# Optimization experiments

Hardware: AMD Instinct MI355X
Metric: run time of the kernel (lower is better)

Reference implementation:

```python
import jax, jax.numpy as jnp
import numpy as np

B, L, H, E = 2, 2048, 16, 64  # self-attention: S=L, D=E


def setup_inputs() -> dict:
    key = jax.random.key(0)
    kq, kk, kv = jax.random.split(key, 3)
    queries = jax.random.normal(kq, (B, L, H, E), dtype=jnp.float32)
    keys = jax.random.normal(kk, (B, L, H, E), dtype=jnp.float32)
    values = jax.random.normal(kv, (B, L, H, E), dtype=jnp.float32)
    return {"queries": queries, "keys": keys, "values": values}


def reference(queries, keys, values):
    # Faithful to source: scale is computed in torch code but never applied.
    # scores: [B, H, L, S]
    scores = jnp.einsum("blhe,bshe->bhls", queries, keys)
    # TriangularCausalMask: triu(ones, diagonal=1) -> mask strictly-future positions
    Lq = queries.shape[1]
    causal = jnp.triu(jnp.ones((Lq, Lq), dtype=bool), k=1)  # [L, S]
    scores = jnp.where(causal[None, None, :, :], -jnp.inf, scores)
    A = jax.nn.softmax(scores, axis=-1)  # dropout in eval mode = identity
    V = jnp.einsum("bhls,bshd->blhd", A, values)
    return V
```

## Files before the change

kernel.cpp:

```cpp
#include <hip/hip_runtime.h>

typedef short bf16x8 __attribute__((ext_vector_type(8)));
typedef short bf16x4 __attribute__((ext_vector_type(4)));
typedef short bf16x2 __attribute__((ext_vector_type(2)));
typedef float f32x4 __attribute__((ext_vector_type(4)));

#define LOG2E 1.4426950408889634f

static __device__ __forceinline__ unsigned short f2bf(float x) {
  unsigned int u = __builtin_bit_cast(unsigned int, x);
  u += 0x7fffu + ((u >> 16) & 1u);
  return (unsigned short)(u >> 16);
}
static __device__ __forceinline__ float bf2f(unsigned short h) {
  unsigned int u = ((unsigned int)h) << 16;
  return __builtin_bit_cast(float, u);
}

static __device__ __forceinline__ void gl_lds16(const void* g, void* l) {
  __builtin_amdgcn_global_load_lds(
      (const __attribute__((address_space(1))) void*)g,
      (__attribute__((address_space(3))) void*)l, 16, 0, 0);
}

__global__ __launch_bounds__(256)
void prep_kv(const float* __restrict__ K, const float* __restrict__ V,
             short* __restrict__ ws) {
  __shared__ float tmp[64 * 65];
  const int isV = blockIdx.x >> 10;
  const int tile = blockIdx.x & 1023;
  const int bh = tile >> 5, kt = tile & 31;
  const int b = bh >> 4, h = bh & 15;
  const int tid = threadIdx.x;
  if (!isV) {
    const float* Kb = K + ((size_t)b * 2048 + kt * 64) * 1024 + h * 64;
    short* ohi = ws + (size_t)tile * 4096;
    short* olo = ws + 4194304 + (size_t)tile * 4096;
    for (int i = 0; i < 2; ++i) {
      const int chunk = tid + 256 * i;
      const int row = chunk >> 3, p = chunk & 7;
      const int c = p ^ (row & 7);
      const float* src = Kb + (size_t)row * 1024 + c * 8;
      const f32x4 a = *(const f32x4*)src;
      const f32x4 d = *(const f32x4*)(src + 4);
      bf16x8 hi, lo;
      for (int j = 0; j < 4; ++j) {
        const unsigned short hb = f2bf(a[j]);
        hi[j] = (short)hb; lo[j] = (short)f2bf(a[j] - bf2f(hb));
      }
      for (int j = 0; j < 4; ++j) {
        const unsigned short hb = f2bf(d[j]);
        hi[4 + j] = (short)hb; lo[4 + j] = (short)f2bf(d[j] - bf2f(hb));
      }
      *(bf16x8*)(ohi + chunk * 8) = hi;
      *(bf16x8*)(olo + chunk * 8) = lo;
    }
  } else {
    const float* Vb = V + ((size_t)b * 2048 + kt * 64) * 1024 + h * 64;
    short* ovt = ws + 8388608 + (size_t)tile * 4096;
    for (int i = 0; i < 4; ++i) {
      const int idx = tid + 256 * i;
      const int row = idx >> 4, c4 = idx & 15;
      const f32x4 v = *(const f32x4*)(Vb + (size_t)row * 1024 + c4 * 4);
      for (int j = 0; j < 4; ++j) tmp[row * 65 + c4 * 4 + j] = v[j];
    }
    __syncthreads();
    for (int i = 0; i < 2; ++i) {
      const int chunk = tid + 256 * i;
      const int e = chunk >> 3, p = chunk & 7;
      const int s0 = (p ^ (e & 7)) * 8;
      bf16x8 o;
      for (int j = 0; j < 8; ++j) o[j] = (short)f2bf(tmp[(s0 + j) * 65 + e]);
      *(bf16x8*)(ovt + chunk * 8) = o;
    }
  }
}

__global__ __launch_bounds__(256, 2)
void fa_fwd2(const float* __restrict__ Qg, const short* __restrict__ ws,
             float* __restrict__ Og) {
  __shared__ short sKhi[2][4096];
  __shared__ short sKlo[2][4096];
  __shared__ short sVt[2][4096];
  __shared__ short sP[4096];

  const int tid = threadIdx.x;
  const int lane = tid & 63;
  const int wv = tid >> 6;
  const int ml = lane & 15, quad = lane >> 4;
  const int bh = blockIdx.x;
  const int b = bh >> 4, h = bh & 15;
  const float* Qb = Qg + (size_t)b * 2048 * 1024 + h * 64;
  float* Ob = Og + (size_t)b * 2048 * 1024 + h * 64;
  const short* wsKhi = ws;
  const short* wsKlo = ws + 4194304;
  const short* wsVt = ws + 8388608;
  const int wrow0 = wv * 16;
  const bf16x8 ones = {16256, 16256, 16256, 16256, 16256, 16256, 16256, 16256};
  const f32x4 vzero = {0.f, 0.f, 0.f, 0.f};

  for (int half = 0; half < 2; ++half) {
    const int qt = half ? 31 - (int)blockIdx.y : (int)blockIdx.y;
    const int qbase = qt * 64;
    const int nkt = qt + 1;

    bf16x8 qhi[2], qlo[2];
    {
      const float* qr = Qb + (size_t)(qbase + wrow0 + ml) * 1024;
      for (int ks = 0; ks < 2; ++ks) {
        const int e0 = ks * 32 + quad * 8;
        const f32x4 a = *(const f32x4*)(qr + e0);
        const f32x4 c4 = *(const f32x4*)(qr + e0 + 4);
        for (int j = 0; j < 4; ++j) {
          const unsigned short hb = f2bf(a[j]);
          qhi[ks][j] = (short)hb;
          qlo[ks][j] = (short)f2bf(a[j] - bf2f(hb));
        }
        for (int j = 0; j < 4; ++j) {
          const unsigned short hb = f2bf(c4[j]);
          qhi[ks][4 + j] = (short)hb;
          qlo[ks][4 + j] = (short)f2bf(c4[j] - bf2f(hb));
        }
      }
    }

    f32x4 acc[4];
    f32x4 accl = vzero;
    for (int et = 0; et < 4; ++et) acc[et] = vzero;

    auto stage = [&](int kt, int bf) {
      const size_t ktile = ((size_t)bh * 32 + kt) * 4096;
      const short* g0 = wsKhi + ktile;
      const short* g1 = wsKlo + ktile;
      const short* g2 = wsVt + ktile;
      const int o0 = tid * 8, o1 = (tid + 256) * 8;
      gl_lds16(g0 + o0, &sKhi[bf][o0]);
      gl_lds16(g0 + o1, &sKhi[bf][o1]);
      gl_lds16(g1 + o0, &sKlo[bf][o0]);
      gl_lds16(g1 + o1, &sKlo[bf][o1]);
      gl_lds16(g2 + o0, &sVt[bf][o0]);
      gl_lds16(g2 + o1, &sVt[bf][o1]);
    };

    stage(0, 0);
    __syncthreads();

    for (int kt = 0; kt < nkt; ++kt) {
      const int buf = kt & 1;
      if (kt + 1 < nkt) stage(kt + 1, buf ^ 1);

      f32x4 S[4];
      for (int nt = 0; nt < 4; ++nt) S[nt] = vzero;
      for (int ks = 0; ks < 2; ++ks) {
        const int ch = (ks << 2) + quad;
        for (int nt = 0; nt < 4; ++nt) {
          const int srow = nt * 16 + ml;
          const int off = srow * 64 + ((ch ^ (srow & 7)) << 3);
          const bf16x8 kh = *(const bf16x8*)(&sKhi[buf][off]);
          const bf16x8 kl = *(const bf16x8*)(&sKlo[buf][off]);
          S[nt] = __builtin_amdgcn_mfma_f32_16x16x32_bf16(qhi[ks], kh, S[nt], 0, 0, 0);
          S[nt] = __builtin_amdgcn_mfma_f32_16x16x32_bf16(qlo[ks], kh, S[nt], 0, 0, 0);
          S[nt] = __builtin_amdgcn_mfma_f32_16x16x32_bf16(qhi[ks], kl, S[nt], 0, 0, 0);
        }
      }

      const bool dg = (kt * 64 + 63) > (qbase + wrow0);
      for (int nt = 0; nt < 4; ++nt)
        for (int r = 0; r < 4; ++r) {
          float p = __builtin_amdgcn_exp2f(S[nt][r] * LOG2E);
          if (dg) {
            const int sg = kt * 64 + nt * 16 + ml;
            const int lg = qbase + wrow0 + quad * 4 + r;
            if (sg > lg) p = 0.f;
          }
          const int pr = wrow0 + quad * 4 + r;
          const int s = nt * 16 + ml;
          sP[pr * 64 + (((s >> 3) ^ (pr & 7)) << 3) + (s & 7)] = (short)f2bf(p);
        }

      for (int ks = 0; ks < 2; ++ks) {
        const int ch = (ks << 2) + quad;
        const int lrow = wrow0 + ml;
        const bf16x8 pa = *(const bf16x8*)(&sP[lrow * 64 + ((ch ^ (lrow & 7)) << 3)]);
        accl = __builtin_amdgcn_mfma_f32_16x16x32_bf16(pa, ones, accl, 0, 0, 0);
        for (int et = 0; et < 4; ++et) {
          const int e = et * 16 + ml;
          const bf16x8 vb = *(const bf16x8*)(&sVt[buf][e * 64 + ((ch ^ (e & 7)) << 3)]);
          acc[et] = __builtin_amdgcn_mfma_f32_16x16x32_bf16(pa, vb, acc[et], 0, 0, 0);
        }
      }
      __syncthreads();
    }

    for (int r = 0; r < 4; ++r) {
      const float inv = 1.0f / accl[r];
      float* orow = Ob + (size_t)(qbase + wrow0 + quad * 4 + r) * 1024;
      for (int et = 0; et < 4; ++et)
        orow[et * 16 + ml] = acc[et][r] * inv;
    }
  }
}

__global__ __launch_bounds__(512, 2)
void fa_fwd_fb(const float* __restrict__ Qg, const float* __restrict__ Kg,
               const float* __restrict__ Vg, float* __restrict__ Og) {
  constexpr int HE = 1024, Lr = 2048;
  __shared__ short sKhi[2][64 * 64];
  __shared__ short sKlo[2][64 * 64];
  __shared__ short sVt[2][64 * 64];
  __shared__ short sP[128 * 64];

  const int tid = threadIdx.x;
  const int lane = tid & 63;
  const int wv = tid >> 6;
  const int ml = lane & 15;
  const int quad = lane >> 4;

  const int b = blockIdx.x >> 4, h = blockIdx.x & 15;
  const size_t headoff = (size_t)b * (size_t)Lr * HE + (size_t)h * 64;
  const float* Qb = Qg + headoff;
  const float* Kb = Kg + headoff;
  const float* Vb = Vg + headoff;
  float* Ob = Og + headoff;

  const f32x4 vzero = {0.f, 0.f, 0.f, 0.f};

  for (int half = 0; half < 2; ++half) {
    const int qt = half ? (15 - (int)blockIdx.y) : (int)blockIdx.y;
    const int qbase = qt * 128;
    const int wrow0 = wv * 16;

    bf16x8 qhi[2], qlo[2];
    {
      const float* qr = Qb + (size_t)(qbase + wrow0 + ml) * HE;
      for (int ks = 0; ks < 2; ++ks) {
        const int e0 = ks * 32 + quad * 8;
        const f32x4 a = *(const f32x4*)(qr + e0);
        const f32x4 c4 = *(const f32x4*)(qr + e0 + 4);
        for (int j = 0; j < 4; ++j) {
          const unsigned short hb = f2bf(a[j]);
          qhi[ks][j] = (short)hb;
          qlo[ks][j] = (short)f2bf(a[j] - bf2f(hb));
        }
        for (int j = 0; j < 4; ++j) {
          const unsigned short hb = f2bf(c4[j]);
          qhi[ks][4 + j] = (short)hb;
          qlo[ks][4 + j] = (short)f2bf(c4[j] - bf2f(hb));
        }
      }
    }

    f32x4 acc[4];
    float mrun[4], lrun[4];
    for (int et = 0; et < 4; ++et) acc[et] = vzero;
    for (int r = 0; r < 4; ++r) { mrun[r] = -1e30f; lrun[r] = 0.f; }

    const int nkt = 2 * qt + 2;
    for (int kt = 0; kt < nkt; ++kt) {
      const int buf = kt & 1;
      for (int i = 0; i < 2; ++i) {
        const int idx = tid + 512 * i;
        const int row = idx >> 4, c = idx & 15;
        const f32x4 kv = *(const f32x4*)(Kb + (size_t)(kt * 64 + row) * HE + c * 4);
        bf16x4 hi, lo;
        for (int j = 0; j < 4; ++j) {
          const unsigned short hb = f2bf(kv[j]);
          hi[j] = (short)hb;
          lo[j] = (short)f2bf(kv[j] - bf2f(hb));
        }
        const int off = row * 64 + (((c >> 1) ^ (row & 7)) << 3) + ((c & 1) << 2);
        *(bf16x4*)(&sKhi[buf][off]) = hi;
        *(bf16x4*)(&sKlo[buf][off]) = lo;
      }
      {
        const int c = tid & 15, rb = tid >> 4;
        const int s0 = rb * 2;
        const f32x4 v0 = *(const f32x4*)(Vb + (size_t)(kt * 64 + s0) * HE + c * 4);
        const f32x4 v1 = *(const f32x4*)(Vb + (size_t)(kt * 64 + s0 + 1) * HE + c * 4);
        for (int j = 0; j < 4; ++j) {
          const int e = c * 4 + j;
          bf16x2 p;
          p[0] = (short)f2bf(v0[j]);
          p[1] = (short)f2bf(v1[j]);
          const int off = e * 64 + (((s0 >> 3) ^ (e & 7)) << 3) + (s0 & 7);
          *(bf16x2*)(&sVt[buf][off]) = p;
        }
      }
      __syncthreads();

      f32x4 S[4];
      for (int nt = 0; nt < 4; ++nt) S[nt] = vzero;
      for (int ks = 0; ks < 2; ++ks) {
        const int ch = (ks << 2) + quad;
        for (int nt = 0; nt < 4; ++nt) {
          const int srow = nt * 16 + ml;
          const int off = srow * 64 + ((ch ^ (srow & 7)) << 3);
          const bf16x8 kh = *(const bf16x8*)(&sKhi[buf][off]);
          const bf16x8 kl = *(const bf16x8*)(&sKlo[buf][off]);
          S[nt] = __builtin_amdgcn_mfma_f32_16x16x32_bf16(qhi[ks], kh, S[nt], 0, 0, 0);
          S[nt] = __builtin_amdgcn_mfma_f32_16x16x32_bf16(qlo[ks], kh, S[nt], 0, 0, 0);
          S[nt] = __builtin_amdgcn_mfma_f32_16x16x32_bf16(qhi[ks], kl, S[nt], 0, 0, 0);
        }
      }

      if (kt * 64 + 63 > qbase + wrow0) {
        for (int nt = 0; nt < 4; ++nt)
          for (int r = 0; r < 4; ++r) {
            const int sg = kt * 64 + nt * 16 + ml;
            const int lg = qbase + wrow0 + quad * 4 + r;
            if (sg > lg) S[nt][r] = -1e30f;
          }
      }

      float mnew[4], al[4], rsum[4];
      for (int r = 0; r < 4; ++r) {
        float mx = fmaxf(fmaxf(S[0][r], S[1][r]), fmaxf(S[2][r], S[3][r]));
        mx = fmaxf(mx, __shfl_xor(mx, 1));
        mx = fmaxf(mx, __shfl_xor(mx, 2));
        mx = fmaxf(mx, __shfl_xor(mx, 4));
        mx = fmaxf(mx, __shfl_xor(mx, 8));
        mnew[r] = fmaxf(mrun[r], mx);
        al[r] = __builtin_amdgcn_exp2f((mrun[r] - mnew[r]) * LOG2E);
        mrun[r] = mnew[r];
        rsum[r] = 0.f;
      }
      for (int nt = 0; nt < 4; ++nt)
        for (int r = 0; r < 4; ++r) {
          const float p = __builtin_amdgcn_exp2f((S[nt][r] - mnew[r]) * LOG2E);
          S[nt][r] = p;
          rsum[r] += p;
        }
      for (int r = 0; r < 4; ++r) {
        rsum[r] += __shfl_xor(rsum[r], 1);
        rsum[r] += __shfl_xor(rsum[r], 2);
        rsum[r] += __shfl_xor(rsum[r], 4);
        rsum[r] += __shfl_xor(rsum[r], 8);
        lrun[r] = lrun[r] * al[r] + rsum[r];
      }
      for (int et = 0; et < 4; ++et)
        for (int r = 0; r < 4; ++r) acc[et][r] *= al[r];

      for (int nt = 0; nt < 4; ++nt)
        for (int r = 0; r < 4; ++r) {
          const int pr = wrow0 + quad * 4 + r;
          const int s = nt * 16 + ml;
          sP[pr * 64 + (((s >> 3) ^ (pr & 7)) << 3) + (s & 7)] = (short)f2bf(S[nt][r]);
        }

      for (int ks = 0; ks < 2; ++ks) {
        const int ch = (ks << 2) + quad;
        const int lrow = wrow0 + ml;
        const bf16x8 pa = *(const bf16x8*)(&sP[lrow * 64 + ((ch ^ (lrow & 7)) << 3)]);
        for (int et = 0; et < 4; ++et) {
          const int e = et * 16 + ml;
          const bf16x8 vb = *(const bf16x8*)(&sVt[buf][e * 64 + ((ch ^ (e & 7)) << 3)]);
          acc[et] = __builtin_amdgcn_mfma_f32_16x16x32_bf16(pa, vb, acc[et], 0, 0, 0);
        }
      }
    }

    for (int r = 0; r < 4; ++r) {
      const float inv = 1.0f / lrun[r];
      float* orow = Ob + (size_t)(qbase + wrow0 + quad * 4 + r) * HE;
      for (int et = 0; et < 4; ++et)
        orow[et * 16 + ml] = acc[et][r] * inv;
    }
  }
}

extern "C" void kernel_launch(void* const* d_in, const int* in_sizes, int n_in,
                              void* d_out, int out_size, void* d_ws, size_t ws_size,
                              hipStream_t stream) {
  const float* Q = (const float*)d_in[0];
  const float* K = (const float*)d_in[1];
  const float* V = (const float*)d_in[2];
  float* O = (float*)d_out;
  if (ws_size >= 25165824u) {
    short* ws = (short*)d_ws;
    hipLaunchKernelGGL(prep_kv, dim3(2048, 1, 1), dim3(256, 1, 1), 0, stream, K, V, ws);
    hipLaunchKernelGGL(fa_fwd2, dim3(32, 16, 1), dim3(256, 1, 1), 0, stream, Q, ws, O);
  } else {
    hipLaunchKernelGGL(fa_fwd_fb, dim3(32, 8, 1), dim3(512, 1, 1), 0, stream, Q, K, V, O);
  }
}
```

Measured before the change: 144.0 us.

## Give each wave two 16-row query tiles and each block one 128-row tile

The new attention kernel assigns one 128-row query tile per block, with each wave computing two 16-row m-tiles. Each K and V fragment read from LDS now feeds twice as many MFMAs, which cuts LDS traffic and halves K/V staging per query row. It drops the old pairing of tiles qt and 31-qt, so per-block work now ranges from 2 to 32 key tiles. With all blocks resident at once, the heaviest blocks may lengthen the critical path. It also doubles the sP scratch buffer and raises register pressure.

```diff
diff --git a/kernel.cpp b/kernel.cpp
--- a/kernel.cpp
+++ b/kernel.cpp
@@ -77,12 +77,12 @@
 }
 
 __global__ __launch_bounds__(256, 2)
-void fa_fwd2(const float* __restrict__ Qg, const short* __restrict__ ws,
+void fa_fwd3(const float* __restrict__ Qg, const short* __restrict__ ws,
              float* __restrict__ Og) {
   __shared__ short sKhi[2][4096];
   __shared__ short sKlo[2][4096];
   __shared__ short sVt[2][4096];
-  __shared__ short sP[4096];
+  __shared__ short sP[8192];
 
   const int tid = threadIdx.x;
   const int lane = tid & 63;
@@ -95,18 +95,155 @@
   const short* wsKhi = ws;
   const short* wsKlo = ws + 4194304;
   const short* wsVt = ws + 8388608;
-  const int wrow0 = wv * 16;
+  const int wrow0 = wv * 32;
   const bf16x8 ones = {16256, 16256, 16256, 16256, 16256, 16256, 16256, 16256};
   const f32x4 vzero = {0.f, 0.f, 0.f, 0.f};
 
+  const int qt = 15 - (int)blockIdx.y;
+  const int qbase = qt * 128;
+  const int nkt = 2 * qt + 2;
+
+  bf16x8 qhi[2][2], qlo[2][2];
+  for (int mt = 0; mt < 2; ++mt) {
+    const float* qr = Qb + (size_t)(qbase + wrow0 + mt * 16 + ml) * 1024;
+    for (int ks = 0; ks < 2; ++ks) {
+      const int e0 = ks * 32 + quad * 8;
+      const f32x4 a = *(const f32x4*)(qr + e0);
+      const f32x4 c4 = *(const f32x4*)(qr + e0 + 4);
+      for (int j = 0; j < 4; ++j) {
+        const unsigned short hb = f2bf(a[j]);
+        qhi[mt][ks][j] = (short)hb;
+        qlo[mt][ks][j] = (short)f2bf(a[j] - bf2f(hb));
+      }
+      for (int j = 0; j < 4; ++j) {
+        const unsigned short hb = f2bf(c4[j]);
+        qhi[mt][ks][4 + j] = (short)hb;
+        qlo[mt][ks][4 + j] = (short)f2bf(c4[j] - bf2f(hb));
+      }
+    }
+  }
+
+  f32x4 acc[2][4];
+  f32x4 accl[2];
+  for (int mt = 0; mt < 2; ++mt) {
+    accl[mt] = vzero;
+    for (int et = 0; et < 4; ++et) acc[mt][et] = vzero;
+  }
+
+  auto stage = [&](int kt, int bf) {
+    const size_t ktile = ((size_t)bh * 32 + kt) * 4096;
+    const short* g0 = wsKhi + ktile;
+    const short* g1 = wsKlo + ktile;
+    const short* g2 = wsVt + ktile;
+    const int o0 = tid * 8, o1 = (tid + 256) * 8;
+    gl_lds16(g0 + o0, &sKhi[bf][o0]);
+    gl_lds16(g0 + o1, &sKhi[bf][o1]);
+    gl_lds16(g1 + o0, &sKlo[bf][o0]);
+    gl_lds16(g1 + o1, &sKlo[bf][o1]);
+    gl_lds16(g2 + o0, &sVt[bf][o0]);
+    gl_lds16(g2 + o1, &sVt[bf][o1]);
+  };
+
+  stage(0, 0);
+  __syncthreads();
+
+  for (int kt = 0; kt < nkt; ++kt) {
+    const int buf = kt & 1;
+    if (kt + 1 < nkt) stage(kt + 1, buf ^ 1);
+
+    f32x4 S[2][4];
+    for (int mt = 0; mt < 2; ++mt)
+      for (int nt = 0; nt < 4; ++nt) S[mt][nt] = vzero;
+    for (int ks = 0; ks < 2; ++ks) {
+      const int ch = (ks << 2) + quad;
+      for (int nt = 0; nt < 4; ++nt) {
+        const int srow = nt * 16 + ml;
+        const int off = srow * 64 + ((ch ^ (srow & 7)) << 3);
+        const bf16x8 kh = *(const bf16x8*)(&sKhi[buf][off]);
+        const bf16x8 kl = *(const bf16x8*)(&sKlo[buf][off]);
+        for (int mt = 0; mt < 2; ++mt) {
+          S[mt][nt] = __builtin_amdgcn_mfma_f32_16x16x32_bf16(qhi[mt][ks], kh, S[mt][nt], 0, 0, 0);
+          S[mt][nt] = __builtin_amdgcn_mfma_f32_16x16x32_bf16(qlo[mt][ks], kh, S[mt][nt], 0, 0, 0);
+          S[mt][nt] = __builtin_amdgcn_mfma_f32_16x16x32_bf16(qhi[mt][ks], kl, S[mt][nt], 0, 0, 0);
+        }
+      }
+    }
+
+    for (int mt = 0; mt < 2; ++mt) {
+      const bool dg = (kt * 64 + 63) > (qbase + wrow0 + mt * 16);
+      for (int nt = 0; nt < 4; ++nt)
+        for (int r = 0; r < 4; ++r) {
+          float p = __builtin_amdgcn_exp2f(S[mt][nt][r] * LOG2E);
+          if (dg) {
+            const int sg = kt * 64 + nt * 16 + ml;
+            const int lg = qbase + wrow0 + mt * 16 + quad * 4 + r;
+            if (sg > lg) p = 0.f;
+          }
+          const int pr = wrow0 + mt * 16 + quad * 4 + r;
+          const int s = nt * 16 + ml;
+          sP[pr * 64 + (((s >> 3) ^ (pr & 7)) << 3) + (s & 7)] = (short)f2bf(p);
+        }
+    }
+
+    for (int ks = 0; ks < 2; ++ks) {
+      const int ch = (ks << 2) + quad;
+      bf16x8 pa[2];
+      for (int mt = 0; mt < 2; ++mt) {
+        const int lrow = wrow0 + mt * 16 + ml;
+        pa[mt] = *(const bf16x8*)(&sP[lrow * 64 + ((ch ^ (lrow & 7)) << 3)]);
+        accl[mt] = __builtin_amdgcn_mfma_f32_16x16x32_bf16(pa[mt], ones, accl[mt], 0, 0, 0);
+      }
+      for (int et = 0; et < 4; ++et) {
+        const int e = et * 16 + ml;
+        const bf16x8 vb = *(const bf16x8*)(&sVt[buf][e * 64 + ((ch ^ (e & 7)) << 3)]);
+        for (int mt = 0; mt < 2; ++mt)
+          acc[mt][et] = __builtin_amdgcn_mfma_f32_16x16x32_bf16(pa[mt], vb, acc[mt][et], 0, 0, 0);
+      }
+    }
+    __syncthreads();
+  }
+
+  for (int mt = 0; mt < 2; ++mt)
+    for (int r = 0; r < 4; ++r) {
+      const float inv = 1.0f / accl[mt][r];
+      float* orow = Ob + (size_t)(qbase + wrow0 + mt * 16 + quad * 4 + r) * 1024;
+      for (int et = 0; et < 4; ++et)
+        orow[et * 16 + ml] = acc[mt][et][r] * inv;
+    }
+}
+
+__global__ __launch_bounds__(512, 2)
+void fa_fwd_fb(const float* __restrict__ Qg, const float* __restrict__ Kg,
+               const float* __restrict__ Vg, float* __restrict__ Og) {
+  constexpr int HE = 1024, Lr = 2048;
+  __shared__ short sKhi[2][64 * 64];
+  __shared__ short sKlo[2][64 * 64];
+  __shared__ short sVt[2][64 * 64];
+  __shared__ short sP[128 * 64];
+
+  const int tid = threadIdx.x;
+  const int lane = tid & 63;
+  const int wv = tid >> 6;
+  const int ml = lane & 15;
+  const int quad = lane >> 4;
+
+  const int b = blockIdx.x >> 4, h = blockIdx.x & 15;
+  const size_t headoff = (size_t)b * (size_t)Lr * HE + (size_t)h * 64;
+  const float* Qb = Qg + headoff;
+  const float* Kb = Kg + headoff;
+  const float* Vb = Vg + headoff;
+  float* Ob = Og + headoff;
+
+  const f32x4 vzero = {0.f, 0.f, 0.f, 0.f};
+
   for (int half = 0; half < 2; ++half) {
-    const int qt = half ? 31 - (int)blockIdx.y : (int)blockIdx.y;
-    const int qbase = qt * 64;
-    const int nkt = qt + 1;
+    const int qt = half ? (15 - (int)blockIdx.y) : (int)blockIdx.y;
+    const int qbase = qt * 128;
+    const int wrow0 = wv * 16;
 
     bf16x8 qhi[2], qlo[2];
     {
-      const float* qr = Qb + (size_t)(qbase + wrow0 + ml) * 1024;
+      const float* qr = Qb + (size_t)(qbase + wrow0 + ml) * HE;
       for (int ks = 0; ks < 2; ++ks) {
         const int e0 = ks * 32 + quad * 8;
         const f32x4 a = *(const f32x4*)(qr + e0);
@@ -125,29 +262,42 @@
     }
 
     f32x4 acc[4];
-    f32x4 accl = vzero;
+    float mrun[4], lrun[4];
     for (int et = 0; et < 4; ++et) acc[et] = vzero;
-
-    auto stage = [&](int kt, int bf) {
-      const size_t ktile = ((size_t)bh * 32 + kt) * 4096;
-      const short* g0 = wsKhi + ktile;
-      const short* g1 = wsKlo + ktile;
-      const short* g2 = wsVt + ktile;
-      const int o0 = tid * 8, o1 = (tid + 256) * 8;
-      gl_lds16(g0 + o0, &sKhi[bf][o0]);
-      gl_lds16(g0 + o1, &sKhi[bf][o1]);
-      gl_lds16(g1 + o0, &sKlo[bf][o0]);
-      gl_lds16(g1 + o1, &sKlo[bf][o1]);
-      gl_lds16(g2 + o0, &sVt[bf][o0]);
-      gl_lds16(g2 + o1, &sVt[bf][o1]);
-    };
-
-    stage(0, 0);
-    __syncthreads();
-
+    for (int r = 0; r < 4; ++r) { mrun[r] = -1e30f; lrun[r] = 0.f; }
+
+    const int nkt = 2 * qt + 2;
     for (int kt = 0; kt < nkt; ++kt) {
       const int buf = kt & 1;
-      if (kt + 1 < nkt) stage(kt + 1, buf ^ 1);
+      for (int i = 0; i < 2; ++i) {
+        const int idx = tid + 512 * i;
+        const int row = idx >> 4, c = idx & 15;
+        const f32x4 kv = *(const f32x4*)(Kb + (size_t)(kt * 64 + row) * HE + c * 4);
+        bf16x4 hi, lo;
+        for (int j = 0; j < 4; ++j) {
+          const unsigned short hb = f2bf(kv[j]);
+          hi[j] = (short)hb;
+          lo[j] = (short)f2bf(kv[j] - bf2f(hb));
+        }
+        const int off = row * 64 + (((c >> 1) ^ (row & 7)) << 3) + ((c & 1) << 2);
+        *(bf16x4*)(&sKhi[buf][off]) = hi;
+        *(bf16x4*)(&sKlo[buf][off]) = lo;
+      }
+      {
+        const int c = tid & 15, rb = tid >> 4;
+        const int s0 = rb * 2;
+        const f32x4 v0 = *(const f32x4*)(Vb + (size_t)(kt * 64 + s0) * HE + c * 4);
+        const f32x4 v1 = *(const f32x4*)(Vb + (size_t)(kt * 64 + s0 + 1) * HE + c * 4);
+        for (int j = 0; j < 4; ++j) {
+          const int e = c * 4 + j;
+          bf16x2 p;
+          p[0] = (short)f2bf(v0[j]);
+          p[1] = (short)f2bf(v1[j]);
+          const int off = e * 64 + (((s0 >> 3) ^ (e & 7)) << 3) + (s0 & 7);
+          *(bf16x2*)(&sVt[buf][off]) = p;
+        }
+      }
+      __syncthreads();
 
       f32x4 S[4];
       for (int nt = 0; nt < 4; ++nt) S[nt] = vzero;
@@ -164,145 +314,6 @@
         }
       }
 
-      const bool dg = (kt * 64 + 63) > (qbase + wrow0);
-      for (int nt = 0; nt < 4; ++nt)
-        for (int r = 0; r < 4; ++r) {
-          float p = __builtin_amdgcn_exp2f(S[nt][r] * LOG2E);
-          if (dg) {
-            const int sg = kt * 64 + nt * 16 + ml;
-            const int lg = qbase + wrow0 + quad * 4 + r;
-            if (sg > lg) p = 0.f;
-          }
-          const int pr = wrow0 + quad * 4 + r;
-          const int s = nt * 16 + ml;
-          sP[pr * 64 + (((s >> 3) ^ (pr & 7)) << 3) + (s & 7)] = (short)f2bf(p);
-        }
-
-      for (int ks = 0; ks < 2; ++ks) {
-        const int ch = (ks << 2) + quad;
-        const int lrow = wrow0 + ml;
-        const bf16x8 pa = *(const bf16x8*)(&sP[lrow * 64 + ((ch ^ (lrow & 7)) << 3)]);
-        accl = __builtin_amdgcn_mfma_f32_16x16x32_bf16(pa, ones, accl, 0, 0, 0);
-        for (int et = 0; et < 4; ++et) {
-          const int e = et * 16 + ml;
-          const bf16x8 vb = *(const bf16x8*)(&sVt[buf][e * 64 + ((ch ^ (e & 7)) << 3)]);
-          acc[et] = __builtin_amdgcn_mfma_f32_16x16x32_bf16(pa, vb, acc[et], 0, 0, 0);
-        }
-      }
-      __syncthreads();
-    }
-
-    for (int r = 0; r < 4; ++r) {
-      const float inv = 1.0f / accl[r];
-      float* orow = Ob + (size_t)(qbase + wrow0 + quad * 4 + r) * 1024;
-      for (int et = 0; et < 4; ++et)
-        orow[et * 16 + ml] = acc[et][r] * inv;
-    }
-  }
-}
-
-__global__ __launch_bounds__(512, 2)
-void fa_fwd_fb(const float* __restrict__ Qg, const float* __restrict__ Kg,
-               const float* __restrict__ Vg, float* __restrict__ Og) {
-  constexpr int HE = 1024, Lr = 2048;
-  __shared__ short sKhi[2][64 * 64];
-  __shared__ short sKlo[2][64 * 64];
-  __shared__ short sVt[2][64 * 64];
-  __shared__ short sP[128 * 64];
-
-  const int tid = threadIdx.x;
-  const int lane = tid & 63;
-  const int wv = tid >> 6;
-  const int ml = lane & 15;
-  const int quad = lane >> 4;
-
-  const int b = blockIdx.x >> 4, h = blockIdx.x & 15;
-  const size_t headoff = (size_t)b * (size_t)Lr * HE + (size_t)h * 64;
-  const float* Qb = Qg + headoff;
-  const float* Kb = Kg + headoff;
-  const float* Vb = Vg + headoff;
-  float* Ob = Og + headoff;
-
-  const f32x4 vzero = {0.f, 0.f, 0.f, 0.f};
-
-  for (int half = 0; half < 2; ++half) {
-    const int qt = half ? (15 - (int)blockIdx.y) : (int)blockIdx.y;
-    const int qbase = qt * 128;
-    const int wrow0 = wv * 16;
-
-    bf16x8 qhi[2], qlo[2];
-    {
-      const float* qr = Qb + (size_t)(qbase + wrow0 + ml) * HE;
-      for (int ks = 0; ks < 2; ++ks) {
-        const int e0 = ks * 32 + quad * 8;
-        const f32x4 a = *(const f32x4*)(qr + e0);
-        const f32x4 c4 = *(const f32x4*)(qr + e0 + 4);
-        for (int j = 0; j < 4; ++j) {
-          const unsigned short hb = f2bf(a[j]);
-          qhi[ks][j] = (short)hb;
-          qlo[ks][j] = (short)f2bf(a[j] - bf2f(hb));
-        }
-        for (int j = 0; j < 4; ++j) {
-          const unsigned short hb = f2bf(c4[j]);
-          qhi[ks][4 + j] = (short)hb;
-          qlo[ks][4 + j] = (short)f2bf(c4[j] - bf2f(hb));
-        }
-      }
-    }
-
-    f32x4 acc[4];
-    float mrun[4], lrun[4];
-    for (int et = 0; et < 4; ++et) acc[et] = vzero;
-    for (int r = 0; r < 4; ++r) { mrun[r] = -1e30f; lrun[r] = 0.f; }
-
-    const int nkt = 2 * qt + 2;
-    for (int kt = 0; kt < nkt; ++kt) {
-      const int buf = kt & 1;
-      for (int i = 0; i < 2; ++i) {
-        const int idx = tid + 512 * i;
-        const int row = idx >> 4, c = idx & 15;
-        const f32x4 kv = *(const f32x4*)(Kb + (size_t)(kt * 64 + row) * HE + c * 4);
-        bf16x4 hi, lo;
-        for (int j = 0; j < 4; ++j) {
-          const unsigned short hb = f2bf(kv[j]);
-          hi[j] = (short)hb;
-          lo[j] = (short)f2bf(kv[j] - bf2f(hb));
-        }
-        const int off = row * 64 + (((c >> 1) ^ (row & 7)) << 3) + ((c & 1) << 2);
-        *(bf16x4*)(&sKhi[buf][off]) = hi;
-        *(bf16x4*)(&sKlo[buf][off]) = lo;
-      }
-      {
-        const int c = tid & 15, rb = tid >> 4;
-        const int s0 = rb * 2;
-        const f32x4 v0 = *(const f32x4*)(Vb + (size_t)(kt * 64 + s0) * HE + c * 4);
-        const f32x4 v1 = *(const f32x4*)(Vb + (size_t)(kt * 64 + s0 + 1) * HE + c * 4);
-        for (int j = 0; j < 4; ++j) {
-          const int e = c * 4 + j;
-          bf16x2 p;
-          p[0] = (short)f2bf(v0[j]);
-          p[1] = (short)f2bf(v1[j]);
-          const int off = e * 64 + (((s0 >> 3) ^ (e & 7)) << 3) + (s0 & 7);
-          *(bf16x2*)(&sVt[buf][off]) = p;
-        }
-      }
-      __syncthreads();
-
-      f32x4 S[4];
-      for (int nt = 0; nt < 4; ++nt) S[nt] = vzero;
-      for (int ks = 0; ks < 2; ++ks) {
-        const int ch = (ks << 2) + quad;
-        for (int nt = 0; nt < 4; ++nt) {
-          const int srow = nt * 16 + ml;
-          const int off = srow * 64 + ((ch ^ (srow & 7)) << 3);
-          const bf16x8 kh = *(const bf16x8*)(&sKhi[buf][off]);
-          const bf16x8 kl = *(const bf16x8*)(&sKlo[buf][off]);
-          S[nt] = __builtin_amdgcn_mfma_f32_16x16x32_bf16(qhi[ks], kh, S[nt], 0, 0, 0);
-          S[nt] = __builtin_amdgcn_mfma_f32_16x16x32_bf16(qlo[ks], kh, S[nt], 0, 0, 0);
-          S[nt] = __builtin_amdgcn_mfma_f32_16x16x32_bf16(qhi[ks], kl, S[nt], 0, 0, 0);
-        }
-      }
-
       if (kt * 64 + 63 > qbase + wrow0) {
         for (int nt = 0; nt < 4; ++nt)
           for (int r = 0; r < 4; ++r) {
@@ -378,7 +389,7 @@
   if (ws_size >= 25165824u) {
     short* ws = (short*)d_ws;
     hipLaunchKernelGGL(prep_kv, dim3(2048, 1, 1), dim3(256, 1, 1), 0, stream, K, V, ws);
-    hipLaunchKernelGGL(fa_fwd2, dim3(32, 16, 1), dim3(256, 1, 1), 0, stream, Q, ws, O);
+    hipLaunchKernelGGL(fa_fwd3, dim3(32, 16, 1), dim3(256, 1, 1), 0, stream, Q, ws, O);
   } else {
     hipLaunchKernelGGL(fa_fwd_fb, dim3(32, 8, 1), dim3(512, 1, 1), 0, stream, Q, K, V, O);
   }
```

Result: slower. 156.6 us (+8.7%).
